# Kernel tuning notes

Measured on AMD Instinct MI355X. Metric: run time of the kernel, lower is better.

Reference implementation:

```python
import jax, jax.numpy as jnp
import numpy as np

EMBED = 256
HEADS = 8
N, L, S = 4, 128, 64


def setup_inputs() -> dict:
    key = jax.random.key(0)
    ks = jax.random.split(key, 9)
    values = jax.random.normal(ks[0], (N, L, S, EMBED), dtype=jnp.float32)
    keys_ = jax.random.normal(ks[1], (N, L, S, EMBED), dtype=jnp.float32)
    query = jax.random.normal(ks[2], (N, L, S, EMBED), dtype=jnp.float32)
    mask = jax.random.randint(ks[3], (N, 1, L, L, 1), 0, 2, dtype=jnp.int32)
    sc = 1.0 / np.sqrt(EMBED)
    Wq = jax.random.normal(ks[4], (EMBED, EMBED), dtype=jnp.float32) * sc
    Wk = jax.random.normal(ks[5], (EMBED, EMBED), dtype=jnp.float32) * sc
    Wv = jax.random.normal(ks[6], (EMBED, EMBED), dtype=jnp.float32) * sc
    Wo = jax.random.normal(ks[7], (HEADS * EMBED, EMBED), dtype=jnp.float32) * (1.0 / np.sqrt(HEADS * EMBED))
    bo = jnp.zeros((EMBED,), dtype=jnp.float32)
    return {"values": values, "keys": keys_, "query": query, "mask": mask,
            "Wq": Wq, "Wk": Wk, "Wv": Wv, "Wo": Wo, "bo": bo}


def reference(values, keys, query, mask, Wq, Wk, Wv, Wo, bo):
    n, q_len, s_len, d = query.shape
    k_len = keys.shape[1]
    h = HEADS
    # Per-head projections share one weight (expand happens BEFORE Linear in
    # the original), so compute each projection once and broadcast over heads.
    q = jnp.einsum('nqsd,de->nqse', query, Wq)   # [N,Q,S,D]
    k = jnp.einsum('nksd,de->nkse', keys, Wk)    # [N,K,S,D]
    v = jnp.einsum('nksd,de->nkse', values, Wv)  # [N,K,S,D]
    # energy: nqshd,nkshd->nhqks ; identical across h pre-mask
    energy = jnp.einsum('nqsd,nksd->nqks', q, k)            # [N,Q,K,S]
    energy = jnp.broadcast_to(energy[:, None], (n, h, q_len, k_len, s_len))
    energy = jnp.where(mask == 0, jnp.float32(-1e20), energy)
    attn = jax.nn.softmax(energy / jnp.sqrt(jnp.float32(d)), axis=3)  # over K
    # out: nhqls,nlshd->nqshd
    out = jnp.einsum('nhqks,nksd->nqshd', attn, v)
    out = out.reshape(n, q_len, s_len, h * d)
    return out @ Wo + bo
```

## Files before the change

### kernel.cpp

```cpp
#include <hip/hip_runtime.h>
#include <hip/hip_bf16.h>


using bf16x4 = __attribute__((ext_vector_type(4))) __bf16;
using bf16x8 = __attribute__((ext_vector_type(8))) __bf16;
using f32x16 = __attribute__((ext_vector_type(16))) float;

#define MFMA32(a, b, c) __builtin_amdgcn_mfma_f32_32x32x16_bf16((a), (b), (c), 0, 0, 0)

__device__ __forceinline__ bf16x8 cvt8(float4 f0, float4 f1) {
  bf16x8 a;
  a[0]=(__bf16)f0.x; a[1]=(__bf16)f0.y; a[2]=(__bf16)f0.z; a[3]=(__bf16)f0.w;
  a[4]=(__bf16)f1.x; a[5]=(__bf16)f1.y; a[6]=(__bf16)f1.z; a[7]=(__bf16)f1.w;
  return a;
}
__device__ __forceinline__ f32x16 zero16() {
  f32x16 z;
#pragma unroll
  for (int j = 0; j < 16; ++j) z[j] = 0.f;
  return z;
}

__global__ __launch_bounds__(512) void prep_pack(
    const float* __restrict__ Wq, const float* __restrict__ Wk,
    const float* __restrict__ Wv, const float* __restrict__ Wo,
    __bf16* __restrict__ mqk, __bf16* __restrict__ mvo) {
  __shared__ float wt[256 * 33];
  const int t = threadIdx.x, lane = t & 63, w = t >> 6;
  const int lq = lane & 31, hl = lane >> 5;
  const int ct = blockIdx.x;
  const bool isV = blockIdx.y != 0;
  if (isV) {
#pragma unroll
    for (int i = 0; i < 16; ++i) {
      int cell = i * 512 + t;
      int e2 = cell >> 5, eol = cell & 31;
      float ssum = 0.f;
#pragma unroll
      for (int h = 0; h < 8; ++h)
        ssum += Wo[((size_t)(h * 256 + e2)) * 256 + ct * 32 + eol];
      wt[e2 * 33 + eol] = ssum;
    }
    __syncthreads();
  }
  const float* Aw = isV ? Wv : Wq;
  bf16x8 afr[16], bfr[16];
#pragma unroll
  for (int ks = 0; ks < 16; ++ks) {
    const float* p = Aw + (size_t)(w * 32 + lq) * 256 + ks * 16 + hl * 8;
    afr[ks] = cvt8(*(const float4*)p, *(const float4*)(p + 4));
  }
  if (!isV) {
#pragma unroll
    for (int ks = 0; ks < 16; ++ks) {
      const float* p = Wk + (size_t)(ct * 32 + lq) * 256 + ks * 16 + hl * 8;
      bfr[ks] = cvt8(*(const float4*)p, *(const float4*)(p + 4));
    }
  } else {
#pragma unroll
    for (int ks = 0; ks < 16; ++ks)
#pragma unroll
      for (int jj = 0; jj < 8; ++jj)
        bfr[ks][jj] = (__bf16)wt[(ks * 16 + hl * 8 + jj) * 33 + lq];
  }
  f32x16 acc = zero16();
#pragma unroll
  for (int ks = 0; ks < 16; ++ks) acc = MFMA32(afr[ks], bfr[ks], acc);
  char* dstb = (char*)(isV ? mvo : mqk);
#pragma unroll
  for (int a = 0; a < 4; ++a) {
    bf16x4 v;
#pragma unroll
    for (int j = 0; j < 4; ++j) v[j] = (__bf16)acc[4 * a + j];
    *(bf16x4*)(dstb + ct * 16384 + (2 * w + (a >> 1)) * 1024 +
               (lq + 32 * (a & 1)) * 16 + hl * 8) = v;
  }
}

__global__ __launch_bounds__(512) void fused_attn(
    const float* __restrict__ Xv, const float* __restrict__ Xk,
    const float* __restrict__ Xq, const int* __restrict__ mask,
    const __bf16* __restrict__ mqk, const __bf16* __restrict__ mvo,
    const float* __restrict__ bo, float* __restrict__ out) {
  extern __shared__ char lds[];
  char* A     = lds;
  char* Timg  = lds + 65536;
  char* Pimg  = lds + 65536;
  char* B1img = lds + 98304;
  float* scr  = (float*)(lds + 98304);
  const int t = threadIdx.x, lane = t & 63, w = t >> 6;
  const int lq = lane & 31, hl = lane >> 5;
  const int qt = w & 3, kh = w >> 2;
  const int sl = blockIdx.x, n = sl >> 6, s = sl & 63;

  auto fill = [&](const float* __restrict__ X, float4* vr) {
#pragma unroll
    for (int i = 0; i < 8; ++i) {
      int f8 = i * 512 + t, row = f8 >> 5, c8 = f8 & 31;
      const float* src = X + ((size_t)(n * 8192 + row * 64 + s)) * 256 + c8 * 8;
      vr[2 * i]     = *reinterpret_cast<const float4*>(src);
      vr[2 * i + 1] = *reinterpret_cast<const float4*>(src + 4);
    }
  };
  auto flushv = [&](const float4* vr) {
#pragma unroll
    for (int i = 0; i < 8; ++i) {
      int f8 = i * 512 + t, row = f8 >> 5, c8 = f8 & 31;
      bf16x8 b;
      b[0]=(__bf16)vr[2*i].x;   b[1]=(__bf16)vr[2*i].y;
      b[2]=(__bf16)vr[2*i].z;   b[3]=(__bf16)vr[2*i].w;
      b[4]=(__bf16)vr[2*i+1].x; b[5]=(__bf16)vr[2*i+1].y;
      b[6]=(__bf16)vr[2*i+1].z; b[7]=(__bf16)vr[2*i+1].w;
      *reinterpret_cast<bf16x8*>(A + row * 512 + ((c8 * 16) ^ ((row & 7) << 4))) = b;
    }
  };
  auto xfrag = [&](int brow, int ks) -> bf16x8 {
    return *reinterpret_cast<const bf16x8*>(
        A + brow * 512 + ((ks * 32 + hl * 16) ^ ((brow & 7) << 4)));
  };

  { float4 vr[16]; fill(Xq, vr); flushv(vr); }
  __syncthreads();

  float4 vrp[16];
  fill(Xk, vrp);
  {
    const bf16x8* wp = reinterpret_cast<const bf16x8*>(mqk);
    bf16x8 wf[16];
#pragma unroll
    for (int ks = 0; ks < 16; ++ks) wf[ks] = wp[(w * 16 + ks) * 64 + lane];
#pragma unroll
    for (int rt = 0; rt < 4; ++rt) {
      f32x16 acc = zero16();
#pragma unroll
      for (int ks = 0; ks < 16; ++ks)
        acc = MFMA32(wf[ks], xfrag(rt * 32 + lq, ks), acc);
#pragma unroll
      for (int a = 0; a < 4; ++a) {
        bf16x4 v;
#pragma unroll
        for (int j = 0; j < 4; ++j) v[j] = (__bf16)acc[4 * a + j];
        *(bf16x4*)(Timg + rt * 16384 + (2 * w + (a >> 1)) * 1024 +
                   (lq + 32 * (a & 1)) * 16 + hl * 8) = v;
      }
    }
  }
  __syncthreads();

  bf16x8 af[16];
#pragma unroll
  for (int ks = 0; ks < 16; ++ks)
    af[ks] = *reinterpret_cast<const bf16x8*>(Timg + qt * 16384 + ks * 1024 + lane * 16);
  flushv(vrp);
  __syncthreads();

  fill(Xv, vrp);
  int ms[2][16];
#pragma unroll
  for (int c = 0; c < 2; ++c)
#pragma unroll
    for (int a = 0; a < 4; ++a) {
      int4 m = *reinterpret_cast<const int4*>(
          mask + ((size_t)n * 128 + qt * 32 + lq) * 128 +
          (2 * kh + c) * 32 + 8 * a + 4 * hl);
      ms[c][4*a] = m.x; ms[c][4*a+1] = m.y; ms[c][4*a+2] = m.z; ms[c][4*a+3] = m.w;
    }
  f32x16 acc[2];
#pragma unroll
  for (int c = 0; c < 2; ++c) {
    acc[c] = zero16();
    int kt = 2 * kh + c;
#pragma unroll
    for (int ks = 0; ks < 16; ++ks)
      acc[c] = MFMA32(xfrag(kt * 32 + lq, ks), af[ks], acc[c]);
  }
  float mx = -3e38f;
#pragma unroll
  for (int c = 0; c < 2; ++c)
#pragma unroll
    for (int r = 0; r < 16; ++r) {
      float sv = ms[c][r] ? acc[c][r] * 0.0625f : -6.25e18f;
      acc[c][r] = sv;
      mx = fmaxf(mx, sv);
    }
  mx = fmaxf(mx, __shfl_xor(mx, 32));
  float sum = 0.f;
#pragma unroll
  for (int c = 0; c < 2; ++c)
#pragma unroll
    for (int r = 0; r < 16; ++r) {
      float e = __expf(acc[c][r] - mx);
      acc[c][r] = e;
      sum += e;
    }
  sum += __shfl_xor(sum, 32);
  if (lane < 32) {
    float2* s2 = reinterpret_cast<float2*>(scr);
    s2[(qt * 2 + kh) * 32 + lane] = make_float2(mx, sum);
  }
  __syncthreads();

  {
    float2 pr = reinterpret_cast<const float2*>(scr)[(qt * 2 + (kh ^ 1)) * 32 + lq];
    float M = fmaxf(mx, pr.x);
    float tot = sum * __expf(mx - M) + pr.y * __expf(pr.x - M);
    float scale = __expf(mx - M) / tot;
#pragma unroll
    for (int c = 0; c < 2; ++c)
#pragma unroll
      for (int r = 0; r < 16; ++r) acc[c][r] *= scale;
  }
#pragma unroll
  for (int c = 0; c < 2; ++c)
#pragma unroll
    for (int a = 0; a < 4; ++a) {
      bf16x4 v;
#pragma unroll
      for (int j = 0; j < 4; ++j) v[j] = (__bf16)acc[c][4 * a + j];
      *(bf16x4*)(Pimg + qt * 8192 + ((2 * kh + c) * 2 + (a >> 1)) * 1024 +
                 (lq + 32 * (a & 1)) * 16 + hl * 8) = v;
    }
  flushv(vrp);
  bf16x8 vf[16];
  {
    const bf16x8* vp = reinterpret_cast<const bf16x8*>(mvo);
#pragma unroll
    for (int ks = 0; ks < 16; ++ks) vf[ks] = vp[(w * 16 + ks) * 64 + lane];
  }
  __syncthreads();

#pragma unroll
  for (int rt = 0; rt < 4; ++rt) {
    f32x16 a1 = zero16();
#pragma unroll
    for (int ks = 0; ks < 16; ++ks)
      a1 = MFMA32(xfrag(rt * 32 + lq, ks), vf[ks], a1);
#pragma unroll
    for (int a = 0; a < 4; ++a) {
      bf16x4 v;
#pragma unroll
      for (int j = 0; j < 4; ++j) v[j] = (__bf16)a1[4 * a + j];
      *(bf16x4*)(B1img + w * 8192 + (2 * rt + (a >> 1)) * 1024 +
                 (lq + 32 * (a & 1)) * 16 + hl * 8) = v;
    }
  }
  __syncthreads();

  bf16x8 pa[8];
#pragma unroll
  for (int ks = 0; ks < 8; ++ks)
    pa[ks] = *reinterpret_cast<const bf16x8*>(Pimg + qt * 8192 + ks * 1024 + lane * 16);
  float* orow = out + ((size_t)(n * 8192) + (qt * 32 + lq) * 64 + s) * 256;
#pragma unroll
  for (int el = 0; el < 4; ++el) {
    int et = kh * 4 + el;
    f32x16 a2 = zero16();
#pragma unroll
    for (int ks = 0; ks < 8; ++ks) {
      bf16x8 bfr = *reinterpret_cast<const bf16x8*>(
          B1img + et * 8192 + ks * 1024 + lane * 16);
      a2 = MFMA32(bfr, pa[ks], a2);
    }
#pragma unroll
    for (int a = 0; a < 4; ++a) {
      float4 bv = *reinterpret_cast<const float4*>(bo + et * 32 + 8 * a + 4 * hl);
      float4 st;
      st.x = a2[4*a]   + bv.x; st.y = a2[4*a+1] + bv.y;
      st.z = a2[4*a+2] + bv.z; st.w = a2[4*a+3] + bv.w;
      *reinterpret_cast<float4*>(orow + et * 32 + 8 * a + 4 * hl) = st;
    }
  }
}

extern "C" void kernel_launch(void* const* d_in, const int* in_sizes, int n_in,
                              void* d_out, int out_size, void* d_ws, size_t ws_size,
                              hipStream_t stream) {
  const float* values = (const float*)d_in[0];
  const float* keys   = (const float*)d_in[1];
  const float* query  = (const float*)d_in[2];
  const int*   mask   = (const int*)d_in[3];
  const float* Wq     = (const float*)d_in[4];
  const float* Wk     = (const float*)d_in[5];
  const float* Wv     = (const float*)d_in[6];
  const float* Wo     = (const float*)d_in[7];
  const float* bo     = (const float*)d_in[8];
  float* out = (float*)d_out;

  char* w = (char*)d_ws;
  __bf16* mqk = (__bf16*)w; w += 131072;
  __bf16* mvo = (__bf16*)w; w += 131072;

  prep_pack<<<dim3(8, 2), 512, 0, stream>>>(Wq, Wk, Wv, Wo, mqk, mvo);
  fused_attn<<<256, 512, 163840, stream>>>(values, keys, query, mask,
                                           mqk, mvo, bo, out);
}
```

Before: 54.13 us.

## Keep V·Wo product in registers, bit-pack mask, build MFMA fragments via shuffles

The mask is packed into 32-bit words in the prep kernel, so the attention kernel reads two words instead of eight int4 loads per lane. The second GEMM stage now keeps each wave's V·Wo tile in registers as MFMA A-fragments, built with cross-half shuffles, instead of writing it to LDS. It then reads P fragments from LDS, which removes the B1img buffer, one barrier and the LDS round trip, and cuts dynamic LDS to 128KB. The Wq·Wk fragment load is also hoisted ahead of the first fill. In exchange it uses more registers and adds shuffles, and the P writes change to full-fragment uint4 stores.

```diff
diff --git a/kernel.cpp b/kernel.cpp
--- a/kernel.cpp
+++ b/kernel.cpp
@@ -20,17 +20,48 @@
   for (int j = 0; j < 16; ++j) z[j] = 0.f;
   return z;
 }
+__device__ __forceinline__ unsigned pk(float a, float b) {
+  union { __bf16 h[2]; unsigned u; } x;
+  x.h[0] = (__bf16)a; x.h[1] = (__bf16)b;
+  return x.u;
+}
+__device__ __forceinline__ bf16x8 u4frag(uint4 w) {
+  union { uint4 u; bf16x8 f; } x;
+  x.u = w;
+  return x.f;
+}
+__device__ __forceinline__ uint4 mkfrag(const float* a8, int hl) {
+  unsigned p00 = pk(a8[0], a8[1]), p01 = pk(a8[2], a8[3]);
+  unsigned p10 = pk(a8[4], a8[5]), p11 = pk(a8[6], a8[7]);
+  unsigned r0 = __shfl_xor((int)(hl ? p00 : p10), 32);
+  unsigned r1 = __shfl_xor((int)(hl ? p01 : p11), 32);
+  uint4 w;
+  w.x = hl ? r0 : p00;  w.y = hl ? r1 : p01;
+  w.z = hl ? p10 : r0;  w.w = hl ? p11 : r1;
+  return w;
+}
 
 __global__ __launch_bounds__(512) void prep_pack(
     const float* __restrict__ Wq, const float* __restrict__ Wk,
     const float* __restrict__ Wv, const float* __restrict__ Wo,
-    __bf16* __restrict__ mqk, __bf16* __restrict__ mvo) {
+    const int* __restrict__ mask,
+    __bf16* __restrict__ mqk, __bf16* __restrict__ mvo,
+    unsigned* __restrict__ mbits) {
   __shared__ float wt[256 * 33];
   const int t = threadIdx.x, lane = t & 63, w = t >> 6;
   const int lq = lane & 31, hl = lane >> 5;
   const int ct = blockIdx.x;
   const bool isV = blockIdx.y != 0;
-  if (isV) {
+  if (!isV) {
+    int gid = ct * 512 + t;
+    if (gid < 2048) {
+      const int* mrow = mask + gid * 32;
+      unsigned mw = 0;
+#pragma unroll
+      for (int b = 0; b < 32; ++b) mw |= (mrow[b] != 0 ? 1u : 0u) << b;
+      mbits[gid] = mw;
+    }
+  } else {
 #pragma unroll
     for (int i = 0; i < 16; ++i) {
       int cell = i * 512 + t;
@@ -79,14 +110,13 @@
 
 __global__ __launch_bounds__(512) void fused_attn(
     const float* __restrict__ Xv, const float* __restrict__ Xk,
-    const float* __restrict__ Xq, const int* __restrict__ mask,
+    const float* __restrict__ Xq, const unsigned* __restrict__ mbits,
     const __bf16* __restrict__ mqk, const __bf16* __restrict__ mvo,
     const float* __restrict__ bo, float* __restrict__ out) {
   extern __shared__ char lds[];
   char* A     = lds;
   char* Timg  = lds + 65536;
   char* Pimg  = lds + 65536;
-  char* B1img = lds + 98304;
   float* scr  = (float*)(lds + 98304);
   const int t = threadIdx.x, lane = t & 63, w = t >> 6;
   const int lq = lane & 31, hl = lane >> 5;
@@ -119,30 +149,30 @@
         A + brow * 512 + ((ks * 32 + hl * 16) ^ ((brow & 7) << 4)));
   };
 
+  bf16x8 wf[16];
+  {
+    const bf16x8* wp = reinterpret_cast<const bf16x8*>(mqk);
+#pragma unroll
+    for (int ks = 0; ks < 16; ++ks) wf[ks] = wp[(w * 16 + ks) * 64 + lane];
+  }
   { float4 vr[16]; fill(Xq, vr); flushv(vr); }
   __syncthreads();
 
   float4 vrp[16];
   fill(Xk, vrp);
-  {
-    const bf16x8* wp = reinterpret_cast<const bf16x8*>(mqk);
-    bf16x8 wf[16];
-#pragma unroll
-    for (int ks = 0; ks < 16; ++ks) wf[ks] = wp[(w * 16 + ks) * 64 + lane];
-#pragma unroll
-    for (int rt = 0; rt < 4; ++rt) {
-      f32x16 acc = zero16();
-#pragma unroll
-      for (int ks = 0; ks < 16; ++ks)
-        acc = MFMA32(wf[ks], xfrag(rt * 32 + lq, ks), acc);
-#pragma unroll
-      for (int a = 0; a < 4; ++a) {
-        bf16x4 v;
-#pragma unroll
-        for (int j = 0; j < 4; ++j) v[j] = (__bf16)acc[4 * a + j];
-        *(bf16x4*)(Timg + rt * 16384 + (2 * w + (a >> 1)) * 1024 +
-                   (lq + 32 * (a & 1)) * 16 + hl * 8) = v;
-      }
+#pragma unroll
+  for (int rt = 0; rt < 4; ++rt) {
+    f32x16 acc = zero16();
+#pragma unroll
+    for (int ks = 0; ks < 16; ++ks)
+      acc = MFMA32(wf[ks], xfrag(rt * 32 + lq, ks), acc);
+#pragma unroll
+    for (int a = 0; a < 4; ++a) {
+      bf16x4 v;
+#pragma unroll
+      for (int j = 0; j < 4; ++j) v[j] = (__bf16)acc[4 * a + j];
+      *(bf16x4*)(Timg + rt * 16384 + (2 * w + (a >> 1)) * 1024 +
+                 (lq + 32 * (a & 1)) * 16 + hl * 8) = v;
     }
   }
   __syncthreads();
@@ -155,16 +185,8 @@
   __syncthreads();
 
   fill(Xv, vrp);
-  int ms[2][16];
-#pragma unroll
-  for (int c = 0; c < 2; ++c)
-#pragma unroll
-    for (int a = 0; a < 4; ++a) {
-      int4 m = *reinterpret_cast<const int4*>(
-          mask + ((size_t)n * 128 + qt * 32 + lq) * 128 +
-          (2 * kh + c) * 32 + 8 * a + 4 * hl);
-      ms[c][4*a] = m.x; ms[c][4*a+1] = m.y; ms[c][4*a+2] = m.z; ms[c][4*a+3] = m.w;
-    }
+  unsigned mw0 = mbits[((size_t)n * 128 + qt * 32 + lq) * 4 + 2 * kh];
+  unsigned mw1 = mbits[((size_t)n * 128 + qt * 32 + lq) * 4 + 2 * kh + 1];
   f32x16 acc[2];
 #pragma unroll
   for (int c = 0; c < 2; ++c) {
@@ -176,13 +198,16 @@
   }
   float mx = -3e38f;
 #pragma unroll
-  for (int c = 0; c < 2; ++c)
+  for (int c = 0; c < 2; ++c) {
+    unsigned mw = c ? mw1 : mw0;
 #pragma unroll
     for (int r = 0; r < 16; ++r) {
-      float sv = ms[c][r] ? acc[c][r] * 0.0625f : -6.25e18f;
+      int bit = (r & 3) + 8 * (r >> 2) + 4 * hl;
+      float sv = ((mw >> bit) & 1u) ? acc[c][r] * 0.0625f : -6.25e18f;
       acc[c][r] = sv;
       mx = fmaxf(mx, sv);
     }
+  }
   mx = fmaxf(mx, __shfl_xor(mx, 32));
   float sum = 0.f;
 #pragma unroll
@@ -211,15 +236,17 @@
       for (int r = 0; r < 16; ++r) acc[c][r] *= scale;
   }
 #pragma unroll
-  for (int c = 0; c < 2; ++c)
-#pragma unroll
-    for (int a = 0; a < 4; ++a) {
-      bf16x4 v;
-#pragma unroll
-      for (int j = 0; j < 4; ++j) v[j] = (__bf16)acc[c][4 * a + j];
-      *(bf16x4*)(Pimg + qt * 8192 + ((2 * kh + c) * 2 + (a >> 1)) * 1024 +
-                 (lq + 32 * (a & 1)) * 16 + hl * 8) = v;
-    }
+  for (int c = 0; c < 2; ++c) {
+    int kt = 2 * kh + c;
+#pragma unroll
+    for (int s16 = 0; s16 < 2; ++s16) {
+      float a8[8];
+#pragma unroll
+      for (int i = 0; i < 8; ++i) a8[i] = acc[c][8 * s16 + i];
+      uint4 wd = mkfrag(a8, hl);
+      *(uint4*)(Pimg + qt * 8192 + (kt * 2 + s16) * 1024 + lane * 16) = wd;
+    }
+  }
   flushv(vrp);
   bf16x8 vf[16];
   {
@@ -229,6 +256,7 @@
   }
   __syncthreads();
 
+  bf16x8 afB1[8];
 #pragma unroll
   for (int rt = 0; rt < 4; ++rt) {
     f32x16 a1 = zero16();
@@ -236,38 +264,31 @@
     for (int ks = 0; ks < 16; ++ks)
       a1 = MFMA32(xfrag(rt * 32 + lq, ks), vf[ks], a1);
 #pragma unroll
+    for (int s16 = 0; s16 < 2; ++s16) {
+      float a8[8];
+#pragma unroll
+      for (int i = 0; i < 8; ++i) a8[i] = a1[8 * s16 + i];
+      afB1[rt * 2 + s16] = u4frag(mkfrag(a8, hl));
+    }
+  }
+
+#pragma unroll
+  for (int q4 = 0; q4 < 4; ++q4) {
+    f32x16 a2 = zero16();
+#pragma unroll
+    for (int ks = 0; ks < 8; ++ks) {
+      bf16x8 pfr = *reinterpret_cast<const bf16x8*>(
+          Pimg + q4 * 8192 + ks * 1024 + lane * 16);
+      a2 = MFMA32(afB1[ks], pfr, a2);
+    }
+    float* orow = out + ((size_t)(n * 8192) + (q4 * 32 + lq) * 64 + s) * 256;
+#pragma unroll
     for (int a = 0; a < 4; ++a) {
-      bf16x4 v;
-#pragma unroll
-      for (int j = 0; j < 4; ++j) v[j] = (__bf16)a1[4 * a + j];
-      *(bf16x4*)(B1img + w * 8192 + (2 * rt + (a >> 1)) * 1024 +
-                 (lq + 32 * (a & 1)) * 16 + hl * 8) = v;
-    }
-  }
-  __syncthreads();
-
-  bf16x8 pa[8];
-#pragma unroll
-  for (int ks = 0; ks < 8; ++ks)
-    pa[ks] = *reinterpret_cast<const bf16x8*>(Pimg + qt * 8192 + ks * 1024 + lane * 16);
-  float* orow = out + ((size_t)(n * 8192) + (qt * 32 + lq) * 64 + s) * 256;
-#pragma unroll
-  for (int el = 0; el < 4; ++el) {
-    int et = kh * 4 + el;
-    f32x16 a2 = zero16();
-#pragma unroll
-    for (int ks = 0; ks < 8; ++ks) {
-      bf16x8 bfr = *reinterpret_cast<const bf16x8*>(
-          B1img + et * 8192 + ks * 1024 + lane * 16);
-      a2 = MFMA32(bfr, pa[ks], a2);
-    }
-#pragma unroll
-    for (int a = 0; a < 4; ++a) {
-      float4 bv = *reinterpret_cast<const float4*>(bo + et * 32 + 8 * a + 4 * hl);
+      float4 bv = *reinterpret_cast<const float4*>(bo + w * 32 + 8 * a + 4 * hl);
       float4 st;
       st.x = a2[4*a]   + bv.x; st.y = a2[4*a+1] + bv.y;
       st.z = a2[4*a+2] + bv.z; st.w = a2[4*a+3] + bv.w;
-      *reinterpret_cast<float4*>(orow + et * 32 + 8 * a + 4 * hl) = st;
+      *reinterpret_cast<float4*>(orow + w * 32 + 8 * a + 4 * hl) = st;
     }
   }
 }
@@ -287,10 +308,11 @@
   float* out = (float*)d_out;
 
   char* w = (char*)d_ws;
-  __bf16* mqk = (__bf16*)w; w += 131072;
-  __bf16* mvo = (__bf16*)w; w += 131072;
-
-  prep_pack<<<dim3(8, 2), 512, 0, stream>>>(Wq, Wk, Wv, Wo, mqk, mvo);
-  fused_attn<<<256, 512, 163840, stream>>>(values, keys, query, mask,
+  __bf16*   mqk   = (__bf16*)w;   w += 131072;
+  __bf16*   mvo   = (__bf16*)w;   w += 131072;
+  unsigned* mbits = (unsigned*)w; w += 8192;
+
+  prep_pack<<<dim3(8, 2), 512, 0, stream>>>(Wq, Wk, Wv, Wo, mask, mqk, mvo, mbits);
+  fused_attn<<<256, 512, 131072, stream>>>(values, keys, query, mbits,
                                            mqk, mvo, bo, out);
 }
```

After: 53.71 us. About the same (-0.8%).
